# Optimization experiments

Hardware: AMD Instinct MI355X
Metric: run time of the kernel (lower is better)

The kernel has to match this reference:

```python
import jax, jax.numpy as jnp
import numpy as np

BITS = 4
MAXQ = (1 << BITS) - 1      # 15
PACK = 32 // BITS           # 8 values per int32 word
GROUP = 128                 # quantization group size along K


def setup_inputs() -> dict:
    key = jax.random.key(0)
    k0, k1, k2, k3 = jax.random.split(key, 4)
    M, K, N = 4096, 4096, 11008
    G = K // GROUP
    x = jax.random.normal(k0, (M, K), dtype=jnp.float32)
    # packed 4-bit weights: full-range random int32 words (each holds 8 nibbles)
    qweight = jax.random.randint(k1, (K // PACK, N), -(2**31), 2**31 - 1, dtype=jnp.int32)
    # packed zero points: (G, N // PACK) int32 words
    qzeros = jax.random.randint(k2, (G, N // PACK), -(2**31), 2**31 - 1, dtype=jnp.int32)
    # group-wise scales (G, N), small positive values as GPTQ produces
    scales = jax.random.uniform(k3, (G, N), dtype=jnp.float32, minval=1e-3, maxval=1e-2)
    # standard GPTQ grouping: consecutive blocks of GROUP rows share a group
    g_idx = (jnp.arange(K) // GROUP).astype(jnp.int32)
    return {"x": x, "qweight": qweight, "scales": scales, "qzeros": qzeros, "g_idx": g_idx}


def _dequant(qweight, scales, qzeros, g_idx):
    """Unpack int32-packed 4-bit weights and dequantize to float. Returns (K, N)."""
    K = g_idx.shape[0]
    N = qweight.shape[1]
    k = jnp.arange(K)
    # nibble k lives in word k//PACK at bit offset (k%PACK)*BITS
    k_shift = ((k % PACK) * BITS).astype(jnp.int32)
    w = (qweight[k // PACK] >> k_shift[:, None]) & MAXQ              # (K, N) int32 in [0, MAXQ]
    n = jnp.arange(N)
    n_shift = ((n % PACK) * BITS).astype(jnp.int32)
    z = ((qzeros[:, n // PACK] >> n_shift[None, :]) & MAXQ) + 1      # (G, N); kernel adds 1
    return (w - z[g_idx]).astype(scales.dtype) * scales[g_idx]       # (K, N) float


def reference(x, qweight, scales, qzeros, g_idx):
    # C = A @ dequant(B), fp32 accumulation as in the Triton kernel
    W = _dequant(qweight, scales, qzeros, g_idx)
    return jnp.matmul(x, W, preferred_element_type=jnp.float32)
```

## Files before the change

### kernel.cpp

```cpp
#include <hip/hip_runtime.h>
#include <hip/hip_bf16.h>
#include <stdint.h>

typedef _Float16 half8 __attribute__((ext_vector_type(8)));
typedef __attribute__((ext_vector_type(8))) short short8;
typedef __attribute__((ext_vector_type(4))) float floatx4;
typedef __attribute__((ext_vector_type(4))) uint32_t uint32x4;

#define GROUP_SZ 128

__device__ __forceinline__ uint32_t cvt_pk_f16(float lo, float hi) {
    uint32_t r;
    asm("v_cvt_pkrtz_f16_f32 %0, %1, %2" : "=v"(r) : "v"(lo), "v"(hi));
    return r;
}
__device__ __forceinline__ uint32_t pk_add_f16(uint32_t a, uint32_t b) {
    uint32_t r;
    asm("v_pk_add_f16 %0, %1, %2" : "=v"(r) : "v"(a), "v"(b));
    return r;
}
__device__ __forceinline__ uint32_t pk_mul_f16(uint32_t a, uint32_t b) {
    uint32_t r;
    asm("v_pk_mul_f16 %0, %1, %2" : "=v"(r) : "v"(a), "v"(b));
    return r;
}

__global__ __launch_bounds__(256)
void convA_kernel(const float* __restrict__ x, uint4* __restrict__ aws, int total8) {
    int idx = blockIdx.x * 256 + threadIdx.x;
    if (idx >= total8) return;
    const float4* xp = reinterpret_cast<const float4*>(x) + (size_t)idx * 2;
    float4 a = xp[0], b = xp[1];
    uint4 o;
    o.x = cvt_pk_f16(a.x, a.y);
    o.y = cvt_pk_f16(a.z, a.w);
    o.z = cvt_pk_f16(b.x, b.y);
    o.w = cvt_pk_f16(b.z, b.w);
    aws[idx] = o;
}

__global__ __launch_bounds__(256)
void deqB_kernel(const int* __restrict__ qw, const float* __restrict__ sc,
                 const int* __restrict__ qz, char* __restrict__ bws, int K, int N) {
    const int n = blockIdx.x * 256 + threadIdx.x;
    const int wk = blockIdx.y;
    if (n >= N) return;
    const uint32_t w = (uint32_t)qw[(size_t)wk * N + n];
    const int g = wk >> 4;
    const float s = sc[(size_t)g * N + n];
    const uint32_t zw = (uint32_t)qz[(size_t)g * (N >> 3) + (n >> 3)];
    const float zf = -(float)(1025u + ((zw >> ((n & 7) * 4)) & 15u));
    const uint32_t c2 = cvt_pk_f16(zf, zf);
    const uint32_t s2 = cvt_pk_f16(s, s);
    uint32_t oo[4];
    #pragma unroll
    for (int i = 0; i < 4; ++i) {
        const uint32_t tt = w >> (8 * i);
        const uint32_t qi = ((tt & 0xFu) | 0x64006400u) | ((tt << 12) & 0xF0000u);
        oo[i] = pk_mul_f16(pk_add_f16(qi, c2), s2);
    }
    uint4 o; o.x = oo[0]; o.y = oo[1]; o.z = oo[2]; o.w = oo[3];
    const int NKT = K >> 6;
    const int nt = n >> 8, h = (n >> 7) & 1, row = n & 127;
    const int kt = wk >> 3, slot = wk & 7;
    size_t off = ((((size_t)nt * NKT + kt) * 2 + h) * 8 + slot) * 2048 + (size_t)row * 16;
    *reinterpret_cast<uint4*>(bws + off) = o;
}

__global__ __launch_bounds__(512, 2)
void gemm8_kernel(const char* __restrict__ Aws, const char* __restrict__ Bws,
                  float* __restrict__ out, int M, int K, int N) {
    __shared__ char smem[65536];

    const int NT = K >> 6;
    const int nbm = M >> 8, nbn = N >> 8;
    const int nwg = nbm * nbn;
    int bid = blockIdx.x;
    int q = nwg >> 3, r = nwg & 7;
    int xcd = bid & 7, lin = bid >> 3;
    int sid = (xcd < r ? xcd * (q + 1) : r * (q + 1) + (xcd - r) * q) + lin;
    const int bm = sid % nbm, bn = sid / nbm;
    const int m0 = bm << 8, n0 = bn << 8;

    const int tid = threadIdx.x;
    const int lane = tid & 63, w = tid >> 6;
    const int wm = w >> 2, wn = w & 3;
    const int fr = lane & 15, hi = lane >> 4;
    const int r8 = lane >> 3, c8 = lane & 7;
    const uint32_t wOff = (uint32_t)w * 2048u;

    const uint32_t K2 = (uint32_t)K * 2;
    const char* aBase = Aws + (size_t)m0 * K2;
    const char* aPtr[2][2];
    #pragma unroll
    for (int h = 0; h < 2; ++h)
        #pragma unroll
        for (int i = 0; i < 2; ++i)
            aPtr[h][i] = aBase + (size_t)((uint32_t)(h * 128 + w * 16 + i * 8 + r8) * K2
                                          + (uint32_t)((c8 ^ r8) * 16));

    const char* bBase = Bws + (size_t)bn * ((size_t)NT * 32768);
    const int nl0 = wn * 64 + fr;
    const char* bP[2];
    #pragma unroll
    for (int kk = 0; kk < 2; ++kk)
        bP[kk] = bBase + (size_t)(((uint32_t)(nl0 >> 7) * 8 + (uint32_t)(kk * 4 + hi)) * 2048u
                                  + (uint32_t)(nl0 & 127) * 16u);

    uint32_t aRdK[2];
    #pragma unroll
    for (int kk = 0; kk < 2; ++kk)
        aRdK[kk] = (uint32_t)(wm * 128 + fr) * 128u
                 + (uint32_t)(((kk * 4 + hi) ^ (fr & 7)) * 16);

    auto stageA = [&](uint32_t cOff) {
        #pragma unroll
        for (int h = 0; h < 2; ++h)
            #pragma unroll
            for (int i = 0; i < 2; ++i) {
                char* dst = smem + (cOff + wOff + (uint32_t)(h * 16384 + i * 1024));
                __builtin_amdgcn_global_load_lds(
                    (const __attribute__((address_space(1))) void*)aPtr[h][i],
                    (__attribute__((address_space(3))) void*)dst, 16, 0, 0);
                aPtr[h][i] += 128;
            }
    };

    floatx4 acc[8][4];
    const floatx4 fz = {0.f, 0.f, 0.f, 0.f};
    #pragma unroll
    for (int i = 0; i < 8; ++i)
        #pragma unroll
        for (int j = 0; j < 4; ++j) acc[i][j] = fz;
    half8 af_a[4][2], af_b[4][2];
    half8 bf_x[2][2], bf_y[2][2];

#define LOAD_AF(AF, QM, ABASE) { _Pragma("unroll") for (int fmi = 0; fmi < 4; ++fmi) { \
    _Pragma("unroll") for (int kk = 0; kk < 2; ++kk) { \
        uint32x4 u = *reinterpret_cast<const uint32x4*>( \
            (ABASE) + aRdK[kk] + (uint32_t)((QM) * 8192 + fmi * 2048)); \
        AF[fmi][kk] = __builtin_bit_cast(half8, u); } } }

#define LOAD_BFG(BF, QN) { _Pragma("unroll") for (int fnj = 0; fnj < 2; ++fnj) { \
    _Pragma("unroll") for (int kk = 0; kk < 2; ++kk) { \
        uint32x4 u = *reinterpret_cast<const uint32x4*>( \
            bP[kk] + (uint32_t)((QN) * 512 + fnj * 256)); \
        BF[fnj][kk] = __builtin_bit_cast(half8, u); } } }

#define ADV_BP() { bP[0] += 32768; bP[1] += 32768; }

#define MM(AF, BF, QM, QN) { _Pragma("unroll") for (int kk = 0; kk < 2; ++kk) \
    _Pragma("unroll") for (int fmi = 0; fmi < 4; ++fmi) \
    _Pragma("unroll") for (int fnj = 0; fnj < 2; ++fnj) \
        acc[(QM) * 4 + fmi][(QN) * 2 + fnj] = __builtin_amdgcn_mfma_f32_16x16x32_f16( \
            AF[fmi][kk], BF[fnj][kk], acc[(QM) * 4 + fmi][(QN) * 2 + fnj], 0, 0, 0); }

    stageA(0);
    if (NT > 1) stageA(32768u);
    LOAD_BFG(bf_x, 0);
    LOAD_BFG(bf_y, 1);
    ADV_BP();
    if (NT > 1) { asm volatile("s_waitcnt vmcnt(12)" ::: "memory"); }
    else        { asm volatile("s_waitcnt vmcnt(8)" ::: "memory"); }
    __builtin_amdgcn_s_barrier();

    for (int t = 0; t < NT; ++t) {
        const uint32_t cOff = (uint32_t)(t & 1) * 32768u;
        const char* As = smem + cOff;
        const bool st1 = (t + 1 < NT);
        const bool st2 = (t + 2 < NT);
        LOAD_AF(af_a, 0, As);
        LOAD_AF(af_b, 1, As);
        __builtin_amdgcn_s_setprio(1);
        MM(af_a, bf_x, 0, 0);
        MM(af_b, bf_x, 1, 0);
        __builtin_amdgcn_s_setprio(0);
        if (st1) LOAD_BFG(bf_x, 0);
        __builtin_amdgcn_s_setprio(1);
        MM(af_a, bf_y, 0, 1);
        MM(af_b, bf_y, 1, 1);
        __builtin_amdgcn_s_setprio(0);
        if (st1) { LOAD_BFG(bf_y, 1); ADV_BP(); }
        __builtin_amdgcn_s_barrier();
        if (st2) {
            stageA(cOff);
            asm volatile("s_waitcnt vmcnt(12)" ::: "memory");
        } else if (st1) {
            asm volatile("s_waitcnt vmcnt(8)" ::: "memory");
        }
        if (st1) __builtin_amdgcn_s_barrier();
    }
#undef LOAD_AF
#undef LOAD_BFG
#undef ADV_BP
#undef MM

    float* op = out + (size_t)(m0 + wm * 128) * N + n0 + wn * 64;
    #pragma unroll
    for (int fm = 0; fm < 8; ++fm)
        #pragma unroll
        for (int fn = 0; fn < 4; ++fn)
            #pragma unroll
            for (int rr = 0; rr < 4; ++rr)
                op[(size_t)(fm * 16 + hi * 4 + rr) * N + fn * 16 + fr] = acc[fm][fn][rr];
}

__device__ __forceinline__ uint32_t cvt_pk_bf16(float lo, float hi) {
    uint32_t r;
    asm("v_cvt_pk_bf16_f32 %0, %1, %2" : "=v"(r) : "v"(lo), "v"(hi));
    return r;
}
__device__ __forceinline__ uint32_t fswz(uint32_t row, uint32_t byte_in_row) {
    return row * 128u + (byte_in_row ^ ((row & 7u) << 4));
}

__global__ __launch_bounds__(256, 2)
void fused128_kernel(const float* __restrict__ x, const int* __restrict__ qweight,
                     const float* __restrict__ scales, const int* __restrict__ qzeros,
                     float* __restrict__ out, int M, int K, int N) {
    __shared__ char smem[32768];
    char* Ald = smem;
    char* Bld = smem + 16384;
    const int nbm = M / 128, nbn = N / 128;
    const int nwg = nbm * nbn;
    int bid = blockIdx.x;
    int q = nwg >> 3, r = nwg & 7;
    int xcd = bid & 7, lin = bid >> 3;
    int sid = (xcd < r ? xcd * (q + 1) : r * (q + 1) + (xcd - r) * q) + lin;
    int bm = sid / nbn, bn = sid % nbn;
    const int m0 = bm * 128, n0 = bn * 128;
    const int t = threadIdx.x;
    const int lane = t & 63, wave = t >> 6;
    const int tm = t >> 4, tk4 = t & 15;
    const int sn = t & 127, kwh = t >> 7;
    const int gn = n0 + sn;
    const int NT = K / 64;
    float4 av[8]; uint32_t qw[4]; float sc; uint32_t zw;
    const float* xp = x + (size_t)(m0 + tm) * K + tk4 * 4;
    const int* qp = qweight + (size_t)(kwh * 4) * N + gn;
    auto load_tile = [&](int ts) {
        const int k0 = ts * 64;
        #pragma unroll
        for (int i = 0; i < 8; ++i)
            av[i] = *reinterpret_cast<const float4*>(xp + (size_t)i * 16 * K + k0);
        const int g = k0 >> 7;
        sc = scales[(size_t)g * N + gn];
        zw = (uint32_t)qzeros[(size_t)g * (N >> 3) + (gn >> 3)];
        const int* qb = qp + (size_t)(k0 >> 3) * N;
        #pragma unroll
        for (int j = 0; j < 4; ++j) qw[j] = (uint32_t)qb[(size_t)j * N];
    };
    const int zsh = (gn & 7) * 4;
    auto write_tile = [&]() {
        #pragma unroll
        for (int i = 0; i < 8; ++i) {
            uint2 p;
            p.x = cvt_pk_bf16(av[i].x, av[i].y);
            p.y = cvt_pk_bf16(av[i].z, av[i].w);
            *reinterpret_cast<uint2*>(Ald + fswz((uint32_t)(i * 16 + tm), (uint32_t)(tk4 * 8))) = p;
        }
        const float z = (float)((zw >> zsh) & 15u) + 1.0f;
        const float nz = -z * sc;
        #pragma unroll
        for (int j = 0; j < 4; ++j) {
            const uint32_t wv = qw[j];
            float f[8];
            #pragma unroll
            for (int e = 0; e < 8; ++e)
                f[e] = fmaf((float)((wv >> (4 * e)) & 15u), sc, nz);
            uint4 p;
            p.x = cvt_pk_bf16(f[0], f[1]); p.y = cvt_pk_bf16(f[2], f[3]);
            p.z = cvt_pk_bf16(f[4], f[5]); p.w = cvt_pk_bf16(f[6], f[7]);
            *reinterpret_cast<uint4*>(Bld + fswz((uint32_t)sn, (uint32_t)((kwh * 4 + j) * 16))) = p;
        }
    };
    floatx4 acc[4][4];
    const floatx4 fz = {0.f, 0.f, 0.f, 0.f};
    #pragma unroll
    for (int i = 0; i < 4; ++i)
        #pragma unroll
        for (int j = 0; j < 4; ++j) acc[i][j] = fz;
    const int wm = (wave >> 1) * 64, wn = (wave & 1) * 64;
    const int fr = lane & 15;
    const int fkb = ((lane >> 4) * 8) * 2;
    auto compute = [&]() {
        #pragma unroll
        for (int kk = 0; kk < 2; ++kk) {
            short8 afv[4], bfv[4];
            #pragma unroll
            for (int i = 0; i < 4; ++i)
                afv[i] = *reinterpret_cast<const short8*>(
                    Ald + fswz((uint32_t)(wm + i * 16 + fr), (uint32_t)(kk * 64 + fkb)));
            #pragma unroll
            for (int i = 0; i < 4; ++i)
                bfv[i] = *reinterpret_cast<const short8*>(
                    Bld + fswz((uint32_t)(wn + i * 16 + fr), (uint32_t)(kk * 64 + fkb)));
            #pragma unroll
            for (int i = 0; i < 4; ++i)
                #pragma unroll
                for (int j = 0; j < 4; ++j)
                    acc[i][j] = __builtin_amdgcn_mfma_f32_16x16x32_bf16(afv[i], bfv[j], acc[i][j], 0, 0, 0);
        }
    };
    load_tile(0);
    write_tile();
    __syncthreads();
    for (int ts = 0; ts < NT; ++ts) {
        if (ts + 1 < NT) load_tile(ts + 1);
        compute();
        __syncthreads();
        if (ts + 1 < NT) write_tile();
        __syncthreads();
    }
    const int fq = lane >> 4;
    float* op = out + (size_t)(m0 + wm) * N + n0 + wn;
    #pragma unroll
    for (int i = 0; i < 4; ++i)
        #pragma unroll
        for (int j = 0; j < 4; ++j)
            #pragma unroll
            for (int rr = 0; rr < 4; ++rr)
                op[(size_t)(i * 16 + fq * 4 + rr) * N + j * 16 + fr] = acc[i][j][rr];
}

extern "C" void kernel_launch(void* const* d_in, const int* in_sizes, int n_in,
                              void* d_out, int out_size, void* d_ws, size_t ws_size,
                              hipStream_t stream) {
    const float* x       = (const float*)d_in[0];
    const int*   qweight = (const int*)d_in[1];
    const float* scales  = (const float*)d_in[2];
    const int*   qzeros  = (const int*)d_in[3];

    const int K = in_sizes[4];
    const int M = in_sizes[0] / K;
    const int G = K / GROUP_SZ;
    const int N = in_sizes[2] / G;
    float* out = (float*)d_out;

    const size_t needA = (size_t)M * K * 2;
    const size_t needB = (size_t)K * (size_t)N * 2;
    const bool ok = (ws_size >= needA + needB) && (M % 256 == 0) && (N % 256 == 0)
                    && (K % 128 == 0) && (N % 8 == 0);
    if (ok) {
        char* aws = (char*)d_ws;
        char* bws = aws + needA;
        const int total8 = M * (K / 8);
        hipLaunchKernelGGL(convA_kernel, dim3((total8 + 255) / 256), dim3(256), 0, stream,
                           x, (uint4*)aws, total8);
        hipLaunchKernelGGL(deqB_kernel, dim3((N + 255) / 256, K / 8), dim3(256), 0, stream,
                           qweight, scales, qzeros, bws, K, N);
        hipLaunchKernelGGL(gemm8_kernel, dim3((M / 256) * (N / 256)), dim3(512), 0, stream,
                           aws, bws, out, M, K, N);
    } else {
        const int nwg = (M / 128) * (N / 128);
        hipLaunchKernelGGL(fused128_kernel, dim3(nwg), dim3(256), 0, stream,
                           x, qweight, scales, qzeros, out, M, K, N);
    }
}
```

Before: 385.2 us.

## Switch GEMM to 32x32x16 MFMA with matching B prepack and A staging layout

Replaces the 16x16x32 f16 MFMA tiling with 32x32x16 MFMA instructions, so each wave computes 4x2 32x32 tiles. The B prepack layout and the A LDS staging layout are reorganized so each lane loads one contiguous 16-byte fragment per k-slice with no XOR swizzle. B fragment loads are interleaved between the four k-slice MFMA batches. Larger MFMAs give fewer instructions and more reuse per operand load, but the unswizzled A layout may cause LDS bank conflicts, and the vmcnt counts were kept while the number of in-flight loads per stage changed.

After: 495.5 us. 1.29x slower.

```diff
diff --git a/kernel.cpp b/kernel.cpp
--- a/kernel.cpp
+++ b/kernel.cpp
@@ -5,6 +5,7 @@
 typedef _Float16 half8 __attribute__((ext_vector_type(8)));
 typedef __attribute__((ext_vector_type(8))) short short8;
 typedef __attribute__((ext_vector_type(4))) float floatx4;
+typedef __attribute__((ext_vector_type(16))) float floatx16;
 typedef __attribute__((ext_vector_type(4))) uint32_t uint32x4;
 
 #define GROUP_SZ 128
@@ -61,9 +62,10 @@
     }
     uint4 o; o.x = oo[0]; o.y = oo[1]; o.z = oo[2]; o.w = oo[3];
     const int NKT = K >> 6;
-    const int nt = n >> 8, h = (n >> 7) & 1, row = n & 127;
-    const int kt = wk >> 3, slot = wk & 7;
-    size_t off = ((((size_t)nt * NKT + kt) * 2 + h) * 8 + slot) * 2048 + (size_t)row * 16;
+    const int n32 = n >> 5, col = n & 31;
+    const int kt = wk >> 3, ks = (wk >> 1) & 3, kh = wk & 1;
+    size_t off = (((size_t)n32 * NKT + kt) * 4 + (size_t)ks) * 1024
+               + (size_t)kh * 512 + (size_t)col * 16;
     *reinterpret_cast<uint4*>(bws + off) = o;
 }
 
@@ -85,80 +87,63 @@
     const int tid = threadIdx.x;
     const int lane = tid & 63, w = tid >> 6;
     const int wm = w >> 2, wn = w & 3;
-    const int fr = lane & 15, hi = lane >> 4;
-    const int r8 = lane >> 3, c8 = lane & 7;
-    const uint32_t wOff = (uint32_t)w * 2048u;
+    const int l31 = lane & 31, hk = lane >> 5;
+    const uint32_t aRd = (uint32_t)lane * 16u;
 
     const uint32_t K2 = (uint32_t)K * 2;
-    const char* aBase = Aws + (size_t)m0 * K2;
-    const char* aPtr[2][2];
-    #pragma unroll
-    for (int h = 0; h < 2; ++h)
-        #pragma unroll
-        for (int i = 0; i < 2; ++i)
-            aPtr[h][i] = aBase + (size_t)((uint32_t)(h * 128 + w * 16 + i * 8 + r8) * K2
-                                          + (uint32_t)((c8 ^ r8) * 16));
-
-    const char* bBase = Bws + (size_t)bn * ((size_t)NT * 32768);
-    const int nl0 = wn * 64 + fr;
+    const char* aPtr[4];
+    #pragma unroll
+    for (int ks = 0; ks < 4; ++ks)
+        aPtr[ks] = Aws + (size_t)(m0 + w * 32 + l31) * K2
+                       + (size_t)(ks * 32 + hk * 16);
+
     const char* bP[2];
     #pragma unroll
-    for (int kk = 0; kk < 2; ++kk)
-        bP[kk] = bBase + (size_t)(((uint32_t)(nl0 >> 7) * 8 + (uint32_t)(kk * 4 + hi)) * 2048u
-                                  + (uint32_t)(nl0 & 127) * 16u);
-
-    uint32_t aRdK[2];
-    #pragma unroll
-    for (int kk = 0; kk < 2; ++kk)
-        aRdK[kk] = (uint32_t)(wm * 128 + fr) * 128u
-                 + (uint32_t)(((kk * 4 + hi) ^ (fr & 7)) * 16);
+    for (int j = 0; j < 2; ++j)
+        bP[j] = Bws + ((size_t)(bn * 8 + wn * 2 + j) * (size_t)NT) * 4096
+                    + (size_t)lane * 16;
 
     auto stageA = [&](uint32_t cOff) {
         #pragma unroll
-        for (int h = 0; h < 2; ++h)
-            #pragma unroll
-            for (int i = 0; i < 2; ++i) {
-                char* dst = smem + (cOff + wOff + (uint32_t)(h * 16384 + i * 1024));
-                __builtin_amdgcn_global_load_lds(
-                    (const __attribute__((address_space(1))) void*)aPtr[h][i],
-                    (__attribute__((address_space(3))) void*)dst, 16, 0, 0);
-                aPtr[h][i] += 128;
-            }
+        for (int ks = 0; ks < 4; ++ks) {
+            char* dst = smem + (cOff + (uint32_t)(w * 4 + ks) * 1024u);
+            __builtin_amdgcn_global_load_lds(
+                (const __attribute__((address_space(1))) void*)aPtr[ks],
+                (__attribute__((address_space(3))) void*)dst, 16, 0, 0);
+            aPtr[ks] += 128;
+        }
     };
 
-    floatx4 acc[8][4];
-    const floatx4 fz = {0.f, 0.f, 0.f, 0.f};
-    #pragma unroll
-    for (int i = 0; i < 8; ++i)
-        #pragma unroll
-        for (int j = 0; j < 4; ++j) acc[i][j] = fz;
-    half8 af_a[4][2], af_b[4][2];
-    half8 bf_x[2][2], bf_y[2][2];
-
-#define LOAD_AF(AF, QM, ABASE) { _Pragma("unroll") for (int fmi = 0; fmi < 4; ++fmi) { \
-    _Pragma("unroll") for (int kk = 0; kk < 2; ++kk) { \
+    floatx16 acc[4][2];
+    #pragma unroll
+    for (int i = 0; i < 4; ++i)
+        #pragma unroll
+        for (int j = 0; j < 2; ++j)
+            #pragma unroll
+            for (int e = 0; e < 16; ++e) acc[i][j][e] = 0.f;
+    half8 af[4][4];
+    half8 bf[2][4];
+
+#define LOAD_AF_ALL(ABASE) { _Pragma("unroll") for (int mt = 0; mt < 4; ++mt) { \
+    _Pragma("unroll") for (int ks = 0; ks < 4; ++ks) { \
         uint32x4 u = *reinterpret_cast<const uint32x4*>( \
-            (ABASE) + aRdK[kk] + (uint32_t)((QM) * 8192 + fmi * 2048)); \
-        AF[fmi][kk] = __builtin_bit_cast(half8, u); } } }
-
-#define LOAD_BFG(BF, QN) { _Pragma("unroll") for (int fnj = 0; fnj < 2; ++fnj) { \
-    _Pragma("unroll") for (int kk = 0; kk < 2; ++kk) { \
-        uint32x4 u = *reinterpret_cast<const uint32x4*>( \
-            bP[kk] + (uint32_t)((QN) * 512 + fnj * 256)); \
-        BF[fnj][kk] = __builtin_bit_cast(half8, u); } } }
-
-#define ADV_BP() { bP[0] += 32768; bP[1] += 32768; }
-
-#define MM(AF, BF, QM, QN) { _Pragma("unroll") for (int kk = 0; kk < 2; ++kk) \
-    _Pragma("unroll") for (int fmi = 0; fmi < 4; ++fmi) \
-    _Pragma("unroll") for (int fnj = 0; fnj < 2; ++fnj) \
-        acc[(QM) * 4 + fmi][(QN) * 2 + fnj] = __builtin_amdgcn_mfma_f32_16x16x32_f16( \
-            AF[fmi][kk], BF[fnj][kk], acc[(QM) * 4 + fmi][(QN) * 2 + fnj], 0, 0, 0); }
+            (ABASE) + aRd + (uint32_t)(((wm * 4 + mt) * 4 + ks) * 1024)); \
+        af[mt][ks] = __builtin_bit_cast(half8, u); } } }
+
+#define LOAD_BF(KS) { _Pragma("unroll") for (int j = 0; j < 2; ++j) { \
+    uint32x4 u = *reinterpret_cast<const uint32x4*>(bP[j] + (KS) * 1024); \
+    bf[j][KS] = __builtin_bit_cast(half8, u); } }
+
+#define ADV_BP() { bP[0] += 4096; bP[1] += 4096; }
+
+#define MMC(KS) { _Pragma("unroll") for (int mt = 0; mt < 4; ++mt) \
+    _Pragma("unroll") for (int j = 0; j < 2; ++j) \
+        acc[mt][j] = __builtin_amdgcn_mfma_f32_32x32x16_f16( \
+            af[mt][KS], bf[j][KS], acc[mt][j], 0, 0, 0); }
 
     stageA(0);
     if (NT > 1) stageA(32768u);
-    LOAD_BFG(bf_x, 0);
-    LOAD_BFG(bf_y, 1);
+    LOAD_BF(0); LOAD_BF(1); LOAD_BF(2); LOAD_BF(3);
     ADV_BP();
     if (NT > 1) { asm volatile("s_waitcnt vmcnt(12)" ::: "memory"); }
     else        { asm volatile("s_waitcnt vmcnt(8)" ::: "memory"); }
@@ -169,18 +154,15 @@
         const char* As = smem + cOff;
         const bool st1 = (t + 1 < NT);
         const bool st2 = (t + 2 < NT);
-        LOAD_AF(af_a, 0, As);
-        LOAD_AF(af_b, 1, As);
-        __builtin_amdgcn_s_setprio(1);
-        MM(af_a, bf_x, 0, 0);
-        MM(af_b, bf_x, 1, 0);
-        __builtin_amdgcn_s_setprio(0);
-        if (st1) LOAD_BFG(bf_x, 0);
-        __builtin_amdgcn_s_setprio(1);
-        MM(af_a, bf_y, 0, 1);
-        MM(af_b, bf_y, 1, 1);
-        __builtin_amdgcn_s_setprio(0);
-        if (st1) { LOAD_BFG(bf_y, 1); ADV_BP(); }
+        LOAD_AF_ALL(As);
+        __builtin_amdgcn_s_setprio(1); MMC(0); __builtin_amdgcn_s_setprio(0);
+        if (st1) LOAD_BF(0);
+        __builtin_amdgcn_s_setprio(1); MMC(1); __builtin_amdgcn_s_setprio(0);
+        if (st1) LOAD_BF(1);
+        __builtin_amdgcn_s_setprio(1); MMC(2); __builtin_amdgcn_s_setprio(0);
+        if (st1) LOAD_BF(2);
+        __builtin_amdgcn_s_setprio(1); MMC(3); __builtin_amdgcn_s_setprio(0);
+        if (st1) { LOAD_BF(3); ADV_BP(); }
         __builtin_amdgcn_s_barrier();
         if (st2) {
             stageA(cOff);
@@ -190,19 +172,21 @@
         }
         if (st1) __builtin_amdgcn_s_barrier();
     }
-#undef LOAD_AF
-#undef LOAD_BFG
+#undef LOAD_AF_ALL
+#undef LOAD_BF
 #undef ADV_BP
-#undef MM
+#undef MMC
 
     float* op = out + (size_t)(m0 + wm * 128) * N + n0 + wn * 64;
     #pragma unroll
-    for (int fm = 0; fm < 8; ++fm)
-        #pragma unroll
-        for (int fn = 0; fn < 4; ++fn)
-            #pragma unroll
-            for (int rr = 0; rr < 4; ++rr)
-                op[(size_t)(fm * 16 + hi * 4 + rr) * N + fn * 16 + fr] = acc[fm][fn][rr];
+    for (int mt = 0; mt < 4; ++mt)
+        #pragma unroll
+        for (int j = 0; j < 2; ++j)
+            #pragma unroll
+            for (int reg = 0; reg < 16; ++reg) {
+                int row = mt * 32 + (reg & 3) + 8 * (reg >> 2) + 4 * hk;
+                op[(size_t)row * N + j * 32 + l31] = acc[mt][j][reg];
+            }
 }
 
 __device__ __forceinline__ uint32_t cvt_pk_bf16(float lo, float hi) {
```

## Shrink GEMM tile to 128x128 with four waves and higher occupancy

Applied to the files above, without the earlier changes.

Replaces the 256x256-tile, 8-wave GEMM with a 128x128-tile, 4-wave kernel that uses half the shared memory and targets four blocks per CU. Each wave now computes 64x64 and the inner loop alternates K halves. The goal is more workgroups and better latency hiding across CUs, at the cost of lower arithmetic intensity and more global and L2 traffic per FLOP.

New measurement: 493.0 us. 1.28x slower.

```diff
diff --git a/kernel.cpp b/kernel.cpp
--- a/kernel.cpp
+++ b/kernel.cpp
@@ -67,50 +67,47 @@
     *reinterpret_cast<uint4*>(bws + off) = o;
 }
 
-__global__ __launch_bounds__(512, 2)
-void gemm8_kernel(const char* __restrict__ Aws, const char* __restrict__ Bws,
+__global__ __launch_bounds__(256, 4)
+void gemm4_kernel(const char* __restrict__ Aws, const char* __restrict__ Bws,
                   float* __restrict__ out, int M, int K, int N) {
-    __shared__ char smem[65536];
+    __shared__ char smem[32768];
 
     const int NT = K >> 6;
-    const int nbm = M >> 8, nbn = N >> 8;
+    const int nbm = M >> 7, nbn = N >> 7;
     const int nwg = nbm * nbn;
     int bid = blockIdx.x;
     int q = nwg >> 3, r = nwg & 7;
     int xcd = bid & 7, lin = bid >> 3;
     int sid = (xcd < r ? xcd * (q + 1) : r * (q + 1) + (xcd - r) * q) + lin;
     const int bm = sid % nbm, bn = sid / nbm;
-    const int m0 = bm << 8, n0 = bn << 8;
+    const int m0 = bm << 7, n0 = bn << 7;
 
     const int tid = threadIdx.x;
     const int lane = tid & 63, w = tid >> 6;
-    const int wm = w >> 2, wn = w & 3;
+    const int wm = w >> 1, wn = w & 1;
     const int fr = lane & 15, hi = lane >> 4;
     const int r8 = lane >> 3, c8 = lane & 7;
-    const uint32_t wOff = (uint32_t)w * 2048u;
 
     const uint32_t K2 = (uint32_t)K * 2;
-    const char* aBase = Aws + (size_t)m0 * K2;
     const char* aPtr[2][2];
     #pragma unroll
     for (int h = 0; h < 2; ++h)
         #pragma unroll
         for (int i = 0; i < 2; ++i)
-            aPtr[h][i] = aBase + (size_t)((uint32_t)(h * 128 + w * 16 + i * 8 + r8) * K2
-                                          + (uint32_t)((c8 ^ r8) * 16));
-
-    const char* bBase = Bws + (size_t)bn * ((size_t)NT * 32768);
-    const int nl0 = wn * 64 + fr;
+            aPtr[h][i] = Aws + (size_t)(m0 + h * 64 + w * 16 + i * 8 + r8) * K2
+                             + (size_t)((c8 ^ r8) * 16);
+
     const char* bP[2];
     #pragma unroll
     for (int kk = 0; kk < 2; ++kk)
-        bP[kk] = bBase + (size_t)(((uint32_t)(nl0 >> 7) * 8 + (uint32_t)(kk * 4 + hi)) * 2048u
-                                  + (uint32_t)(nl0 & 127) * 16u);
+        bP[kk] = Bws + ((size_t)(bn >> 1) * (size_t)NT) * 32768
+                     + (size_t)((bn & 1) * 16384)
+                     + (size_t)((kk * 4 + hi) * 2048 + wn * 1024 + fr * 16);
 
     uint32_t aRdK[2];
     #pragma unroll
     for (int kk = 0; kk < 2; ++kk)
-        aRdK[kk] = (uint32_t)(wm * 128 + fr) * 128u
+        aRdK[kk] = (uint32_t)(wm * 64 + fr) * 128u
                  + (uint32_t)(((kk * 4 + hi) ^ (fr & 7)) * 16);
 
     auto stageA = [&](uint32_t cOff) {
@@ -118,7 +115,7 @@
         for (int h = 0; h < 2; ++h)
             #pragma unroll
             for (int i = 0; i < 2; ++i) {
-                char* dst = smem + (cOff + wOff + (uint32_t)(h * 16384 + i * 1024));
+                char* dst = smem + (cOff + (uint32_t)(h * 8192 + w * 2048 + i * 1024));
                 __builtin_amdgcn_global_load_lds(
                     (const __attribute__((address_space(1))) void*)aPtr[h][i],
                     (__attribute__((address_space(3))) void*)dst, 16, 0, 0);
@@ -126,61 +123,51 @@
             }
     };
 
-    floatx4 acc[8][4];
+    floatx4 acc[4][4];
     const floatx4 fz = {0.f, 0.f, 0.f, 0.f};
     #pragma unroll
-    for (int i = 0; i < 8; ++i)
+    for (int i = 0; i < 4; ++i)
         #pragma unroll
         for (int j = 0; j < 4; ++j) acc[i][j] = fz;
-    half8 af_a[4][2], af_b[4][2];
-    half8 bf_x[2][2], bf_y[2][2];
-
-#define LOAD_AF(AF, QM, ABASE) { _Pragma("unroll") for (int fmi = 0; fmi < 4; ++fmi) { \
-    _Pragma("unroll") for (int kk = 0; kk < 2; ++kk) { \
-        uint32x4 u = *reinterpret_cast<const uint32x4*>( \
-            (ABASE) + aRdK[kk] + (uint32_t)((QM) * 8192 + fmi * 2048)); \
-        AF[fmi][kk] = __builtin_bit_cast(half8, u); } } }
-
-#define LOAD_BFG(BF, QN) { _Pragma("unroll") for (int fnj = 0; fnj < 2; ++fnj) { \
-    _Pragma("unroll") for (int kk = 0; kk < 2; ++kk) { \
-        uint32x4 u = *reinterpret_cast<const uint32x4*>( \
-            bP[kk] + (uint32_t)((QN) * 512 + fnj * 256)); \
-        BF[fnj][kk] = __builtin_bit_cast(half8, u); } } }
+    half8 af[4];
+    half8 bfA[4], bfB[4];
+
+#define LOAD_AF(KK, ABASE) { _Pragma("unroll") for (int fmi = 0; fmi < 4; ++fmi) { \
+    uint32x4 u = *reinterpret_cast<const uint32x4*>( \
+        (ABASE) + aRdK[KK] + (uint32_t)(fmi * 2048)); \
+    af[fmi] = __builtin_bit_cast(half8, u); } }
+
+#define LOAD_BFG(BF, KK) { _Pragma("unroll") for (int fnj = 0; fnj < 4; ++fnj) { \
+    uint32x4 u = *reinterpret_cast<const uint32x4*>(bP[KK] + (uint32_t)(fnj * 256)); \
+    BF[fnj] = __builtin_bit_cast(half8, u); } }
 
 #define ADV_BP() { bP[0] += 32768; bP[1] += 32768; }
 
-#define MM(AF, BF, QM, QN) { _Pragma("unroll") for (int kk = 0; kk < 2; ++kk) \
-    _Pragma("unroll") for (int fmi = 0; fmi < 4; ++fmi) \
-    _Pragma("unroll") for (int fnj = 0; fnj < 2; ++fnj) \
-        acc[(QM) * 4 + fmi][(QN) * 2 + fnj] = __builtin_amdgcn_mfma_f32_16x16x32_f16( \
-            AF[fmi][kk], BF[fnj][kk], acc[(QM) * 4 + fmi][(QN) * 2 + fnj], 0, 0, 0); }
+#define MM(BF) { _Pragma("unroll") for (int fmi = 0; fmi < 4; ++fmi) \
+    _Pragma("unroll") for (int fnj = 0; fnj < 4; ++fnj) \
+        acc[fmi][fnj] = __builtin_amdgcn_mfma_f32_16x16x32_f16( \
+            af[fmi], BF[fnj], acc[fmi][fnj], 0, 0, 0); }
 
     stageA(0);
-    if (NT > 1) stageA(32768u);
-    LOAD_BFG(bf_x, 0);
-    LOAD_BFG(bf_y, 1);
+    LOAD_BFG(bfA, 0);
+    LOAD_BFG(bfB, 1);
     ADV_BP();
-    if (NT > 1) { asm volatile("s_waitcnt vmcnt(12)" ::: "memory"); }
-    else        { asm volatile("s_waitcnt vmcnt(8)" ::: "memory"); }
+    if (NT > 1) stageA(16384u);
+    if (NT > 1) { asm volatile("s_waitcnt vmcnt(4)" ::: "memory"); }
+    else        { asm volatile("s_waitcnt vmcnt(0)" ::: "memory"); }
     __builtin_amdgcn_s_barrier();
 
     for (int t = 0; t < NT; ++t) {
-        const uint32_t cOff = (uint32_t)(t & 1) * 32768u;
+        const uint32_t cOff = (uint32_t)(t & 1) * 16384u;
         const char* As = smem + cOff;
         const bool st1 = (t + 1 < NT);
         const bool st2 = (t + 2 < NT);
-        LOAD_AF(af_a, 0, As);
-        LOAD_AF(af_b, 1, As);
-        __builtin_amdgcn_s_setprio(1);
-        MM(af_a, bf_x, 0, 0);
-        MM(af_b, bf_x, 1, 0);
-        __builtin_amdgcn_s_setprio(0);
-        if (st1) LOAD_BFG(bf_x, 0);
-        __builtin_amdgcn_s_setprio(1);
-        MM(af_a, bf_y, 0, 1);
-        MM(af_b, bf_y, 1, 1);
-        __builtin_amdgcn_s_setprio(0);
-        if (st1) { LOAD_BFG(bf_y, 1); ADV_BP(); }
+        LOAD_AF(0, As);
+        __builtin_amdgcn_s_setprio(1); MM(bfA); __builtin_amdgcn_s_setprio(0);
+        if (st1) LOAD_BFG(bfA, 0);
+        LOAD_AF(1, As);
+        __builtin_amdgcn_s_setprio(1); MM(bfB); __builtin_amdgcn_s_setprio(0);
+        if (st1) { LOAD_BFG(bfB, 1); ADV_BP(); }
         __builtin_amdgcn_s_barrier();
         if (st2) {
             stageA(cOff);
@@ -195,9 +182,9 @@
 #undef ADV_BP
 #undef MM
 
-    float* op = out + (size_t)(m0 + wm * 128) * N + n0 + wn * 64;
-    #pragma unroll
-    for (int fm = 0; fm < 8; ++fm)
+    float* op = out + (size_t)(m0 + wm * 64) * N + n0 + wn * 64;
+    #pragma unroll
+    for (int fm = 0; fm < 4; ++fm)
         #pragma unroll
         for (int fn = 0; fn < 4; ++fn)
             #pragma unroll
@@ -339,7 +326,7 @@
 
     const size_t needA = (size_t)M * K * 2;
     const size_t needB = (size_t)K * (size_t)N * 2;
-    const bool ok = (ws_size >= needA + needB) && (M % 256 == 0) && (N % 256 == 0)
+    const bool ok = (ws_size >= needA + needB) && (M % 128 == 0) && (N % 256 == 0)
                     && (K % 128 == 0) && (N % 8 == 0);
     if (ok) {
         char* aws = (char*)d_ws;
@@ -349,7 +336,7 @@
                            x, (uint4*)aws, total8);
         hipLaunchKernelGGL(deqB_kernel, dim3((N + 255) / 256, K / 8), dim3(256), 0, stream,
                            qweight, scales, qzeros, bws, K, N);
-        hipLaunchKernelGGL(gemm8_kernel, dim3((M / 256) * (N / 256)), dim3(512), 0, stream,
+        hipLaunchKernelGGL(gemm4_kernel, dim3((M / 128) * (N / 128)), dim3(256), 0, stream,
                            aws, bws, out, M, K, N);
     } else {
         const int nwg = (M / 128) * (N / 128);
```
